# Kernel tuning notes

Measured on AMD Instinct MI355X. Metric: run time of the kernel, lower is better.

Reference implementation:

```python
import jax, jax.numpy as jnp
import numpy as np

B, S, D, H = 2, 2048, 1024, 16
HD = D // H
DFF = 4096
EPS = 1e-5


def layernorm(x, w, b):
    m = jnp.mean(x, axis=-1, keepdims=True)
    v = jnp.mean((x - m) ** 2, axis=-1, keepdims=True)
    return (x - m) / jnp.sqrt(v + EPS) * w + b


def setup_inputs() -> dict:
    key = jax.random.key(0)
    ks = jax.random.split(key, 5)
    s = 0.02  # init scale for weights
    return {
        "src": jax.random.normal(ks[0], (B, S, D), jnp.float32),
        "norm_w": jnp.ones((D,), jnp.float32),
        "norm_b": jnp.zeros((D,), jnp.float32),
        "wqkv_w": jax.random.normal(ks[1], (D, 3 * D), jnp.float32) * s,
        "wqkv_b": jnp.zeros((3 * D,), jnp.float32),
        "out_w": jax.random.normal(ks[2], (D, D), jnp.float32) * s,
        "out_b": jnp.zeros((D,), jnp.float32),
        "fnorm_w": jnp.ones((D,), jnp.float32),
        "fnorm_b": jnp.zeros((D,), jnp.float32),
        "ff1_w": jax.random.normal(ks[3], (D, DFF), jnp.float32) * s,
        "ff1_b": jnp.zeros((DFF,), jnp.float32),
        "ff2_w": jax.random.normal(ks[4], (DFF, D), jnp.float32) * s,
        "ff2_b": jnp.zeros((D,), jnp.float32),
    }


def reference(src, norm_w, norm_b, wqkv_w, wqkv_b, out_w, out_b,
              fnorm_w, fnorm_b, ff1_w, ff1_b, ff2_w, ff2_b):
    bs, seq, dim = src.shape
    hd = dim // H
    qkv = layernorm(src, norm_w, norm_b) @ wqkv_w + wqkv_b  # [b,s,3d]
    qkv = qkv.reshape(bs, seq, 3, H, hd).transpose(2, 0, 3, 1, 4)  # [3,b,h,s,hd]
    q, k, v = qkv[0], qkv[1], qkv[2]
    # ALiBi bias: (j - i) * 2^{-h}, -inf above diagonal (causal)
    i = jnp.arange(seq)[:, None]
    j = jnp.arange(seq)[None, :]
    slopes = 2.0 ** (-jnp.arange(H, dtype=jnp.float32))  # [h]
    rel = (j - i).astype(jnp.float32)  # [s,s]
    bias = slopes[:, None, None] * rel[None]  # [h,s,s]
    bias = jnp.where((j > i)[None], -jnp.inf, bias)
    scale = 1.0 / jnp.sqrt(jnp.asarray(hd, jnp.float32))
    scores = jnp.einsum("bhqd,bhkd->bhqk", q, k) * scale + bias[None]
    attn = jax.nn.softmax(scores, axis=-1)
    ctx = jnp.einsum("bhqk,bhkd->bhqd", attn, v)
    ctx = ctx.transpose(0, 2, 1, 3).reshape(bs, seq, dim)
    src = src + ctx @ out_w + out_b
    h = layernorm(src, fnorm_w, fnorm_b)
    ff = jax.nn.relu(h @ ff1_w + ff1_b) @ ff2_w + ff2_b
    return src + ff
```

## Files before the change

kernel.cpp:

```cpp
#include <hip/hip_runtime.h>
#include <math.h>

#define S_   2048
#define D_   1024
#define H_   16
#define DFF_ 4096

#define NEGINF (-__builtin_huge_valf())

typedef __bf16 bf16x8 __attribute__((ext_vector_type(8)));
typedef float  f32x4  __attribute__((ext_vector_type(4)));

static __device__ __forceinline__ unsigned short f2bf_rne(float f) {
    unsigned int u = __float_as_uint(f);
    u = (u + 0x7fffu + ((u >> 16) & 1u)) >> 16;
    return (unsigned short)u;
}

template<bool OBF>
__global__ __launch_bounds__(256) void ln_kernel(
    const float* __restrict__ x, const float* __restrict__ w,
    const float* __restrict__ b, void* __restrict__ y)
{
    const int row = blockIdx.x;
    const int t = threadIdx.x;
    const float4 v = reinterpret_cast<const float4*>(x + (size_t)row * D_)[t];
    float s  = v.x + v.y + v.z + v.w;
    float ss = v.x*v.x + v.y*v.y + v.z*v.z + v.w*v.w;
    #pragma unroll
    for (int o = 32; o; o >>= 1) {
        s  += __shfl_xor(s,  o, 64);
        ss += __shfl_xor(ss, o, 64);
    }
    __shared__ float red[8];
    const int wid = t >> 6, lane = t & 63;
    if (lane == 0) { red[wid] = s; red[4 + wid] = ss; }
    __syncthreads();
    s  = red[0] + red[1] + red[2] + red[3];
    ss = red[4] + red[5] + red[6] + red[7];
    const float mean = s * (1.f / D_);
    const float var  = ss * (1.f / D_) - mean * mean;
    const float rstd = rsqrtf(var + 1e-5f);
    const float4 wv = reinterpret_cast<const float4*>(w)[t];
    const float4 bv = reinterpret_cast<const float4*>(b)[t];
    float4 o;
    o.x = (v.x - mean) * rstd * wv.x + bv.x;
    o.y = (v.y - mean) * rstd * wv.y + bv.y;
    o.z = (v.z - mean) * rstd * wv.z + bv.z;
    o.w = (v.w - mean) * rstd * wv.w + bv.w;
    if (OBF) {
        ushort4 o4;
        o4.x = f2bf_rne(o.x); o4.y = f2bf_rne(o.y);
        o4.z = f2bf_rne(o.z); o4.w = f2bf_rne(o.w);
        reinterpret_cast<ushort4*>((unsigned short*)y + (size_t)row * D_)[t] = o4;
    } else {
        reinterpret_cast<float4*>((float*)y + (size_t)row * D_)[t] = o;
    }
}

__global__ __launch_bounds__(256) void wcast_kernel(
    const float* __restrict__ in, unsigned short* __restrict__ outT, int K, int N)
{
    __shared__ float t[64][65];
    const int n0 = blockIdx.x * 64, k0 = blockIdx.y * 64;
    const int tid = threadIdx.x;
    #pragma unroll
    for (int i = 0; i < 16; ++i) {
        const int idx = i * 256 + tid;
        const int kk = idx >> 6, nn = idx & 63;
        t[kk][nn] = in[(size_t)(k0 + kk) * N + n0 + nn];
    }
    __syncthreads();
    #pragma unroll
    for (int i = 0; i < 16; ++i) {
        const int idx = i * 256 + tid;
        const int nn = idx >> 6, kk = idx & 63;
        outT[(size_t)(n0 + nn) * K + k0 + kk] = f2bf_rne(t[kk][nn]);
    }
}

template<int EPI, bool OBF>
__global__ __launch_bounds__(256) void bgemm_kernel(
    const __bf16* __restrict__ A,
    const __bf16* __restrict__ Bt,
    const float* __restrict__ bias, const float* __restrict__ res,
    void* __restrict__ Cv, int M, int N, int K)
{
    __shared__ __align__(16) __bf16 As[128 * 64];
    __shared__ __align__(16) __bf16 Bs[128 * 64];
    const int tid  = threadIdx.x;
    const int w    = tid >> 6, lane = tid & 63;
    const int wr   = w >> 1, wc = w & 1;

    const int nwg  = gridDim.x;
    const int lin  = blockIdx.x;
    const int wg   = (lin & 7) * (nwg >> 3) + (lin >> 3);
    const int gridN = N >> 7;
    const int row0 = (wg / gridN) << 7;
    const int col0 = (wg % gridN) << 7;

    const int srow = lane >> 3;
    const int scol = ((lane & 7) ^ srow) << 3;
    const int frow = lane & 15;
    const int l4   = lane >> 4;
    const int r7   = frow & 7;

    f32x4 acc[4][4] = {};

    for (int kt = 0; kt < K; kt += 64) {
        #pragma unroll
        for (int it = 0; it < 4; ++it) {
            const int arow = w * 32 + it * 8;
            __builtin_amdgcn_global_load_lds(
                (__attribute__((address_space(1))) void*)(A + (size_t)(row0 + arow + srow) * K + kt + scol),
                (__attribute__((address_space(3))) void*)(&As[arow * 64]), 16, 0, 0);
            __builtin_amdgcn_global_load_lds(
                (__attribute__((address_space(1))) void*)(Bt + (size_t)(col0 + arow + srow) * K + kt + scol),
                (__attribute__((address_space(3))) void*)(&Bs[arow * 64]), 16, 0, 0);
        }
        __syncthreads();
        #pragma unroll
        for (int kk = 0; kk < 2; ++kk) {
            const int ch = ((kk * 4 + l4) ^ r7) * 8;
            bf16x8 af[4], bfr[4];
            #pragma unroll
            for (int i = 0; i < 4; ++i) {
                af[i]  = *(const bf16x8*)&As[(wr * 64 + i * 16 + frow) * 64 + ch];
                bfr[i] = *(const bf16x8*)&Bs[(wc * 64 + i * 16 + frow) * 64 + ch];
            }
            #pragma unroll
            for (int mi = 0; mi < 4; ++mi)
                #pragma unroll
                for (int ni = 0; ni < 4; ++ni)
                    acc[mi][ni] = __builtin_amdgcn_mfma_f32_16x16x32_bf16(
                        af[mi], bfr[ni], acc[mi][ni], 0, 0, 0);
        }
        __syncthreads();
    }

    float bz[4];
    #pragma unroll
    for (int ni = 0; ni < 4; ++ni) bz[ni] = bias[col0 + wc * 64 + ni * 16 + frow];
    #pragma unroll
    for (int mi = 0; mi < 4; ++mi) {
        #pragma unroll
        for (int j = 0; j < 4; ++j) {
            const int row = row0 + wr * 64 + mi * 16 + l4 * 4 + j;
            #pragma unroll
            for (int ni = 0; ni < 4; ++ni) {
                const int col = col0 + wc * 64 + ni * 16 + frow;
                float v = acc[mi][ni][j] + bz[ni];
                if (EPI == 1) v = fmaxf(v, 0.f);
                if (EPI == 2) v += res[(size_t)row * N + col];
                if (OBF) ((unsigned short*)Cv)[(size_t)row * N + col] = f2bf_rne(v);
                else     ((float*)Cv)[(size_t)row * N + col] = v;
            }
        }
    }
}

__global__ __launch_bounds__(256) void attn_kernel(
    const __bf16* __restrict__ qkv, __bf16* __restrict__ ctx)
{
    const int pair = blockIdx.x & 15;
    const int bh   = blockIdx.x >> 4;
    const int b    = bh >> 4, h = bh & 15;
    const int tid  = threadIdx.x;
    const int wid  = tid >> 6, lane = tid & 63;
    const int l15  = lane & 15, l4 = lane >> 4;
    const float slope = exp2f(-(float)h);
    const size_t rowb = (size_t)b * S_;

    __shared__ __align__(16) __bf16 Ks[64 * 72];
    __shared__ __align__(16) __bf16 Vt[64 * 72];
    __shared__ __align__(16) __bf16 Ps[4 * 16 * 72];

    const int jr = tid >> 3;
    const int c  = tid & 7;
    const int c8 = c * 8;
    __bf16* psw = &Ps[wid * 16 * 72];
    const __bf16* base = qkv + rowb * 3072 + h * 64;

    #pragma unroll 1
    for (int half = 0; half < 2; ++half) {
        const int qt = half ? 31 - pair : pair;
        const int i0 = qt << 6;

        bf16x8 qf[2];
        {
            const __bf16* qp = base + (size_t)(i0 + wid * 16 + l15) * 3072 + l4 * 8;
            qf[0] = *(const bf16x8*)(qp);
            qf[1] = *(const bf16x8*)(qp + 32);
        }

        float m[4], l[4];
        f32x4 acc[4];
        #pragma unroll
        for (int j = 0; j < 4; ++j) { m[j] = NEGINF; l[j] = 0.f; }
        #pragma unroll
        for (int ni = 0; ni < 4; ++ni) acc[ni] = (f32x4){0.f, 0.f, 0.f, 0.f};

        bf16x8 k0, k1, v0, v1;
        {
            const __bf16* kvp = base + (size_t)jr * 3072;
            k0 = *(const bf16x8*)(kvp + 1024 + c8);
            v0 = *(const bf16x8*)(kvp + 2048 + c8);
            k1 = *(const bf16x8*)(kvp + 32 * 3072 + 1024 + c8);
            v1 = *(const bf16x8*)(kvp + 32 * 3072 + 2048 + c8);
        }

        for (int kt = 0; kt <= qt; ++kt) {
            __syncthreads();
            *(bf16x8*)&Ks[jr * 72 + c8]        = k0;
            *(bf16x8*)&Ks[(jr + 32) * 72 + c8] = k1;
            const int sw0 = (((jr >> 3) ^ c) & 7) * 8 + (jr & 7);
            const int sw1 = ((((jr + 32) >> 3) ^ c) & 7) * 8 + (jr & 7);
            #pragma unroll
            for (int e = 0; e < 8; ++e) {
                Vt[(c8 + e) * 72 + sw0] = v0[e];
                Vt[(c8 + e) * 72 + sw1] = v1[e];
            }
            __syncthreads();

            if (kt < qt) {
                const __bf16* kvp = base + (size_t)(((kt + 1) << 6) + jr) * 3072;
                k0 = *(const bf16x8*)(kvp + 1024 + c8);
                v0 = *(const bf16x8*)(kvp + 2048 + c8);
                k1 = *(const bf16x8*)(kvp + 32 * 3072 + 1024 + c8);
                v1 = *(const bf16x8*)(kvp + 32 * 3072 + 2048 + c8);
            }

            f32x4 sf[4];
            #pragma unroll
            for (int ni = 0; ni < 4; ++ni) sf[ni] = (f32x4){0.f, 0.f, 0.f, 0.f};
            #pragma unroll
            for (int kd = 0; kd < 2; ++kd)
                #pragma unroll
                for (int ni = 0; ni < 4; ++ni) {
                    const bf16x8 bf = *(const bf16x8*)&Ks[(ni * 16 + l15) * 72 + kd * 32 + l4 * 8];
                    sf[ni] = __builtin_amdgcn_mfma_f32_16x16x32_bf16(qf[kd], bf, sf[ni], 0, 0, 0);
                }

            float pv[4][4];
            const int j0 = kt << 6;
            if (kt == qt) {
                #pragma unroll
                for (int ni = 0; ni < 4; ++ni) {
                    const int jcol = ni * 16 + l15;
                    #pragma unroll
                    for (int j = 0; j < 4; ++j) {
                        const int iloc = wid * 16 + l4 * 4 + j;
                        pv[ni][j] = (jcol <= iloc)
                            ? fmaf(slope, (float)(jcol - iloc), sf[ni][j] * 0.125f)
                            : NEGINF;
                    }
                }
            } else {
                const float dbase = (float)(j0 - i0);
                #pragma unroll
                for (int ni = 0; ni < 4; ++ni) {
                    const int jcol = ni * 16 + l15;
                    #pragma unroll
                    for (int j = 0; j < 4; ++j) {
                        const int iloc = wid * 16 + l4 * 4 + j;
                        pv[ni][j] = fmaf(slope, dbase + (float)(jcol - iloc), sf[ni][j] * 0.125f);
                    }
                }
            }

            #pragma unroll
            for (int j = 0; j < 4; ++j) {
                float mx = fmaxf(fmaxf(pv[0][j], pv[1][j]), fmaxf(pv[2][j], pv[3][j]));
                mx = fmaxf(mx, __shfl_xor(mx, 1, 64));
                mx = fmaxf(mx, __shfl_xor(mx, 2, 64));
                mx = fmaxf(mx, __shfl_xor(mx, 4, 64));
                mx = fmaxf(mx, __shfl_xor(mx, 8, 64));
                const float mnew = fmaxf(m[j], mx);
                const float corr = __expf(m[j] - mnew);
                float s0 = 0.f;
                #pragma unroll
                for (int ni = 0; ni < 4; ++ni) {
                    const float e = __expf(pv[ni][j] - mnew);
                    pv[ni][j] = e;
                    s0 += e;
                }
                s0 += __shfl_xor(s0, 1, 64);
                s0 += __shfl_xor(s0, 2, 64);
                s0 += __shfl_xor(s0, 4, 64);
                s0 += __shfl_xor(s0, 8, 64);
                l[j] = l[j] * corr + s0;
                m[j] = mnew;
                #pragma unroll
                for (int ni = 0; ni < 4; ++ni) acc[ni][j] *= corr;
            }

            #pragma unroll
            for (int ni = 0; ni < 4; ++ni)
                #pragma unroll
                for (int j = 0; j < 4; ++j)
                    psw[(l4 * 4 + j) * 72 + ni * 16 + l15] = (__bf16)pv[ni][j];
            asm volatile("" ::: "memory");

            #pragma unroll
            for (int kk = 0; kk < 2; ++kk) {
                const bf16x8 pa = *(const bf16x8*)&psw[l15 * 72 + kk * 32 + l4 * 8];
                #pragma unroll
                for (int ni = 0; ni < 4; ++ni) {
                    const int d = ni * 16 + l15;
                    const int pc = ((kk * 4 + l4) ^ (d >> 3)) & 7;
                    const bf16x8 bv = *(const bf16x8*)&Vt[d * 72 + pc * 8];
                    acc[ni] = __builtin_amdgcn_mfma_f32_16x16x32_bf16(pa, bv, acc[ni], 0, 0, 0);
                }
            }
        }

        #pragma unroll
        for (int ni = 0; ni < 4; ++ni) {
            const int col = h * 64 + ni * 16 + l15;
            #pragma unroll
            for (int j = 0; j < 4; ++j) {
                const int row = i0 + wid * 16 + l4 * 4 + j;
                ctx[(rowb + row) * (size_t)D_ + col] = (__bf16)(acc[ni][j] / l[j]);
            }
        }
    }
}

extern "C" void kernel_launch(void* const* d_in, const int* in_sizes, int n_in,
                              void* d_out, int out_size, void* d_ws, size_t ws_size,
                              hipStream_t stream) {
    const float* src     = (const float*)d_in[0];
    const float* norm_w  = (const float*)d_in[1];
    const float* norm_b  = (const float*)d_in[2];
    const float* wqkv_w  = (const float*)d_in[3];
    const float* wqkv_b  = (const float*)d_in[4];
    const float* out_w   = (const float*)d_in[5];
    const float* out_b   = (const float*)d_in[6];
    const float* fnorm_w = (const float*)d_in[7];
    const float* fnorm_b = (const float*)d_in[8];
    const float* ff1_w   = (const float*)d_in[9];
    const float* ff1_b   = (const float*)d_in[10];
    const float* ff2_w   = (const float*)d_in[11];
    const float* ff2_b   = (const float*)d_in[12];
    float* out = (float*)d_out;

    const int M = 2 * S_;
    const size_t MB = 1u << 20;
    char* W = (char*)d_ws;
    unsigned short* wqkvT = (unsigned short*)(W);
    unsigned short* outT  = (unsigned short*)(W + 6  * MB);
    unsigned short* ff1T  = (unsigned short*)(W + 8  * MB);
    unsigned short* ff2T  = (unsigned short*)(W + 16 * MB);
    unsigned short* h1    = (unsigned short*)(W + 24 * MB);
    unsigned short* qkv   = (unsigned short*)(W + 32 * MB);
    unsigned short* ctx   = (unsigned short*)(W + 24 * MB);
    unsigned short* h2    = (unsigned short*)(W + 32 * MB);
    unsigned short* ffmid = (unsigned short*)(W + 40 * MB);
    float*          src2  = (float*)        (W + 80 * MB);

    wcast_kernel<<<dim3(3072/64, 1024/64), 256, 0, stream>>>(wqkv_w, wqkvT, 1024, 3072);
    wcast_kernel<<<dim3(1024/64, 1024/64), 256, 0, stream>>>(out_w,  outT,  1024, 1024);
    wcast_kernel<<<dim3(4096/64, 1024/64), 256, 0, stream>>>(ff1_w,  ff1T,  1024, 4096);
    wcast_kernel<<<dim3(1024/64, 4096/64), 256, 0, stream>>>(ff2_w,  ff2T,  4096, 1024);

    ln_kernel<true><<<M, 256, 0, stream>>>(src, norm_w, norm_b, h1);
    bgemm_kernel<0, true><<<(3072/128) * (M/128), 256, 0, stream>>>(
        (const __bf16*)h1, (const __bf16*)wqkvT, wqkv_b, nullptr, qkv, M, 3072, 1024);
    attn_kernel<<<2 * H_ * 16, 256, 0, stream>>>((const __bf16*)qkv, (__bf16*)ctx);
    bgemm_kernel<2, false><<<(1024/128) * (M/128), 256, 0, stream>>>(
        (const __bf16*)ctx, (const __bf16*)outT, out_b, src, src2, M, 1024, 1024);
    ln_kernel<true><<<M, 256, 0, stream>>>(src2, fnorm_w, fnorm_b, h2);
    bgemm_kernel<1, true><<<(4096/128) * (M/128), 256, 0, stream>>>(
        (const __bf16*)h2, (const __bf16*)ff1T, ff1_b, nullptr, ffmid, M, 4096, 1024);
    bgemm_kernel<2, false><<<(1024/128) * (M/128), 256, 0, stream>>>(
        (const __bf16*)ffmid, (const __bf16*)ff2T, ff2_b, src2, out, M, 1024, 4096);
}
```

Before: 411.1 us.

## Double-buffer GEMM LDS tiles and split attention into one block per query tile

The GEMM now uses two LDS buffers and prefetches the next K tile with global_load_lds while computing on the current one, with a single barrier per iteration. Tile assignment now walks down M first, which changes L2 reuse of weight columns. Attention drops the paired-tile loop and launches 1024 blocks, one per query tile, ordered with the longest causal tiles first to improve load balance and occupancy. Double buffering doubles LDS use per GEMM block (64KB), which may lower occupancy.

```diff
diff --git a/kernel.cpp b/kernel.cpp
--- a/kernel.cpp
+++ b/kernel.cpp
@@ -86,8 +86,8 @@
     const float* __restrict__ bias, const float* __restrict__ res,
     void* __restrict__ Cv, int M, int N, int K)
 {
-    __shared__ __align__(16) __bf16 As[128 * 64];
-    __shared__ __align__(16) __bf16 Bs[128 * 64];
+    __shared__ __align__(16) __bf16 As[2][128 * 64];
+    __shared__ __align__(16) __bf16 Bs[2][128 * 64];
     const int tid  = threadIdx.x;
     const int w    = tid >> 6, lane = tid & 63;
     const int wr   = w >> 1, wc = w & 1;
@@ -95,9 +95,9 @@
     const int nwg  = gridDim.x;
     const int lin  = blockIdx.x;
     const int wg   = (lin & 7) * (nwg >> 3) + (lin >> 3);
-    const int gridN = N >> 7;
-    const int row0 = (wg / gridN) << 7;
-    const int col0 = (wg % gridN) << 7;
+    const int gridM = M >> 7;
+    const int col0 = (wg / gridM) << 7;
+    const int row0 = (wg % gridM) << 7;
 
     const int srow = lane >> 3;
     const int scol = ((lane & 7) ^ srow) << 3;
@@ -105,28 +105,39 @@
     const int l4   = lane >> 4;
     const int r7   = frow & 7;
 
+    const __bf16* Abase = A  + (size_t)(row0 + srow) * K + scol;
+    const __bf16* Bbase = Bt + (size_t)(col0 + srow) * K + scol;
+
     f32x4 acc[4][4] = {};
-
-    for (int kt = 0; kt < K; kt += 64) {
-        #pragma unroll
-        for (int it = 0; it < 4; ++it) {
-            const int arow = w * 32 + it * 8;
-            __builtin_amdgcn_global_load_lds(
-                (__attribute__((address_space(1))) void*)(A + (size_t)(row0 + arow + srow) * K + kt + scol),
-                (__attribute__((address_space(3))) void*)(&As[arow * 64]), 16, 0, 0);
-            __builtin_amdgcn_global_load_lds(
-                (__attribute__((address_space(1))) void*)(Bt + (size_t)(col0 + arow + srow) * K + kt + scol),
-                (__attribute__((address_space(3))) void*)(&Bs[arow * 64]), 16, 0, 0);
-        }
+    const int nt = K >> 6;
+
+#define STAGE_G(bufi, kt)                                                              \
+    _Pragma("unroll")                                                                  \
+    for (int it = 0; it < 4; ++it) {                                                   \
+        const int arow = w * 32 + it * 8;                                              \
+        __builtin_amdgcn_global_load_lds(                                              \
+            (__attribute__((address_space(1))) void*)(Abase + (size_t)arow * K + (kt)),\
+            (__attribute__((address_space(3))) void*)(&As[bufi][arow * 64]), 16, 0, 0);\
+        __builtin_amdgcn_global_load_lds(                                              \
+            (__attribute__((address_space(1))) void*)(Bbase + (size_t)arow * K + (kt)),\
+            (__attribute__((address_space(3))) void*)(&Bs[bufi][arow * 64]), 16, 0, 0);\
+    }
+
+    STAGE_G(0, 0)
+    int buf = 0;
+    for (int t = 0; t < nt; ++t) {
         __syncthreads();
+        if (t + 1 < nt) {
+            STAGE_G(buf ^ 1, (t + 1) << 6)
+        }
         #pragma unroll
         for (int kk = 0; kk < 2; ++kk) {
             const int ch = ((kk * 4 + l4) ^ r7) * 8;
             bf16x8 af[4], bfr[4];
             #pragma unroll
             for (int i = 0; i < 4; ++i) {
-                af[i]  = *(const bf16x8*)&As[(wr * 64 + i * 16 + frow) * 64 + ch];
-                bfr[i] = *(const bf16x8*)&Bs[(wc * 64 + i * 16 + frow) * 64 + ch];
+                af[i]  = *(const bf16x8*)&As[buf][(wr * 64 + i * 16 + frow) * 64 + ch];
+                bfr[i] = *(const bf16x8*)&Bs[buf][(wc * 64 + i * 16 + frow) * 64 + ch];
             }
             #pragma unroll
             for (int mi = 0; mi < 4; ++mi)
@@ -135,8 +146,9 @@
                     acc[mi][ni] = __builtin_amdgcn_mfma_f32_16x16x32_bf16(
                         af[mi], bfr[ni], acc[mi][ni], 0, 0, 0);
         }
-        __syncthreads();
-    }
+        buf ^= 1;
+    }
+#undef STAGE_G
 
     float bz[4];
     #pragma unroll
@@ -162,8 +174,8 @@
 __global__ __launch_bounds__(256) void attn_kernel(
     const __bf16* __restrict__ qkv, __bf16* __restrict__ ctx)
 {
-    const int pair = blockIdx.x & 15;
-    const int bh   = blockIdx.x >> 4;
+    const int bh   = blockIdx.x & 31;
+    const int qt   = 31 - (blockIdx.x >> 5);
     const int b    = bh >> 4, h = bh & 15;
     const int tid  = threadIdx.x;
     const int wid  = tid >> 6, lane = tid & 63;
@@ -181,147 +193,143 @@
     __bf16* psw = &Ps[wid * 16 * 72];
     const __bf16* base = qkv + rowb * 3072 + h * 64;
 
-    #pragma unroll 1
-    for (int half = 0; half < 2; ++half) {
-        const int qt = half ? 31 - pair : pair;
-        const int i0 = qt << 6;
-
-        bf16x8 qf[2];
-        {
-            const __bf16* qp = base + (size_t)(i0 + wid * 16 + l15) * 3072 + l4 * 8;
-            qf[0] = *(const bf16x8*)(qp);
-            qf[1] = *(const bf16x8*)(qp + 32);
-        }
-
-        float m[4], l[4];
-        f32x4 acc[4];
-        #pragma unroll
-        for (int j = 0; j < 4; ++j) { m[j] = NEGINF; l[j] = 0.f; }
-        #pragma unroll
-        for (int ni = 0; ni < 4; ++ni) acc[ni] = (f32x4){0.f, 0.f, 0.f, 0.f};
-
-        bf16x8 k0, k1, v0, v1;
-        {
-            const __bf16* kvp = base + (size_t)jr * 3072;
+    const int i0 = qt << 6;
+
+    bf16x8 qf[2];
+    {
+        const __bf16* qp = base + (size_t)(i0 + wid * 16 + l15) * 3072 + l4 * 8;
+        qf[0] = *(const bf16x8*)(qp);
+        qf[1] = *(const bf16x8*)(qp + 32);
+    }
+
+    float m[4], l[4];
+    f32x4 acc[4];
+    #pragma unroll
+    for (int j = 0; j < 4; ++j) { m[j] = NEGINF; l[j] = 0.f; }
+    #pragma unroll
+    for (int ni = 0; ni < 4; ++ni) acc[ni] = (f32x4){0.f, 0.f, 0.f, 0.f};
+
+    bf16x8 k0, k1, v0, v1;
+    {
+        const __bf16* kvp = base + (size_t)jr * 3072;
+        k0 = *(const bf16x8*)(kvp + 1024 + c8);
+        v0 = *(const bf16x8*)(kvp + 2048 + c8);
+        k1 = *(const bf16x8*)(kvp + 32 * 3072 + 1024 + c8);
+        v1 = *(const bf16x8*)(kvp + 32 * 3072 + 2048 + c8);
+    }
+
+    for (int kt = 0; kt <= qt; ++kt) {
+        __syncthreads();
+        *(bf16x8*)&Ks[jr * 72 + c8]        = k0;
+        *(bf16x8*)&Ks[(jr + 32) * 72 + c8] = k1;
+        const int sw0 = (((jr >> 3) ^ c) & 7) * 8 + (jr & 7);
+        const int sw1 = ((((jr + 32) >> 3) ^ c) & 7) * 8 + (jr & 7);
+        #pragma unroll
+        for (int e = 0; e < 8; ++e) {
+            Vt[(c8 + e) * 72 + sw0] = v0[e];
+            Vt[(c8 + e) * 72 + sw1] = v1[e];
+        }
+        __syncthreads();
+
+        if (kt < qt) {
+            const __bf16* kvp = base + (size_t)(((kt + 1) << 6) + jr) * 3072;
             k0 = *(const bf16x8*)(kvp + 1024 + c8);
             v0 = *(const bf16x8*)(kvp + 2048 + c8);
             k1 = *(const bf16x8*)(kvp + 32 * 3072 + 1024 + c8);
             v1 = *(const bf16x8*)(kvp + 32 * 3072 + 2048 + c8);
         }
 
-        for (int kt = 0; kt <= qt; ++kt) {
-            __syncthreads();
-            *(bf16x8*)&Ks[jr * 72 + c8]        = k0;
-            *(bf16x8*)&Ks[(jr + 32) * 72 + c8] = k1;
-            const int sw0 = (((jr >> 3) ^ c) & 7) * 8 + (jr & 7);
-            const int sw1 = ((((jr + 32) >> 3) ^ c) & 7) * 8 + (jr & 7);
-            #pragma unroll
-            for (int e = 0; e < 8; ++e) {
-                Vt[(c8 + e) * 72 + sw0] = v0[e];
-                Vt[(c8 + e) * 72 + sw1] = v1[e];
-            }
-            __syncthreads();
-
-            if (kt < qt) {
-                const __bf16* kvp = base + (size_t)(((kt + 1) << 6) + jr) * 3072;
-                k0 = *(const bf16x8*)(kvp + 1024 + c8);
-                v0 = *(const bf16x8*)(kvp + 2048 + c8);
-                k1 = *(const bf16x8*)(kvp + 32 * 3072 + 1024 + c8);
-                v1 = *(const bf16x8*)(kvp + 32 * 3072 + 2048 + c8);
-            }
-
-            f32x4 sf[4];
-            #pragma unroll
-            for (int ni = 0; ni < 4; ++ni) sf[ni] = (f32x4){0.f, 0.f, 0.f, 0.f};
-            #pragma unroll
-            for (int kd = 0; kd < 2; ++kd)
+        f32x4 sf[4];
+        #pragma unroll
+        for (int ni = 0; ni < 4; ++ni) sf[ni] = (f32x4){0.f, 0.f, 0.f, 0.f};
+        #pragma unroll
+        for (int kd = 0; kd < 2; ++kd)
+            #pragma unroll
+            for (int ni = 0; ni < 4; ++ni) {
+                const bf16x8 bf = *(const bf16x8*)&Ks[(ni * 16 + l15) * 72 + kd * 32 + l4 * 8];
+                sf[ni] = __builtin_amdgcn_mfma_f32_16x16x32_bf16(qf[kd], bf, sf[ni], 0, 0, 0);
+            }
+
+        float pv[4][4];
+        const int j0 = kt << 6;
+        if (kt == qt) {
+            #pragma unroll
+            for (int ni = 0; ni < 4; ++ni) {
+                const int jcol = ni * 16 + l15;
                 #pragma unroll
-                for (int ni = 0; ni < 4; ++ni) {
-                    const bf16x8 bf = *(const bf16x8*)&Ks[(ni * 16 + l15) * 72 + kd * 32 + l4 * 8];
-                    sf[ni] = __builtin_amdgcn_mfma_f32_16x16x32_bf16(qf[kd], bf, sf[ni], 0, 0, 0);
+                for (int j = 0; j < 4; ++j) {
+                    const int iloc = wid * 16 + l4 * 4 + j;
+                    pv[ni][j] = (jcol <= iloc)
+                        ? fmaf(slope, (float)(jcol - iloc), sf[ni][j] * 0.125f)
+                        : NEGINF;
                 }
-
-            float pv[4][4];
-            const int j0 = kt << 6;
-            if (kt == qt) {
+            }
+        } else {
+            const float dbase = (float)(j0 - i0);
+            #pragma unroll
+            for (int ni = 0; ni < 4; ++ni) {
+                const int jcol = ni * 16 + l15;
                 #pragma unroll
-                for (int ni = 0; ni < 4; ++ni) {
-                    const int jcol = ni * 16 + l15;
-                    #pragma unroll
-                    for (int j = 0; j < 4; ++j) {
-                        const int iloc = wid * 16 + l4 * 4 + j;
-                        pv[ni][j] = (jcol <= iloc)
-                            ? fmaf(slope, (float)(jcol - iloc), sf[ni][j] * 0.125f)
-                            : NEGINF;
-                    }
+                for (int j = 0; j < 4; ++j) {
+                    const int iloc = wid * 16 + l4 * 4 + j;
+                    pv[ni][j] = fmaf(slope, dbase + (float)(jcol - iloc), sf[ni][j] * 0.125f);
                 }
-            } else {
-                const float dbase = (float)(j0 - i0);
-                #pragma unroll
-                for (int ni = 0; ni < 4; ++ni) {
-                    const int jcol = ni * 16 + l15;
-                    #pragma unroll
-                    for (int j = 0; j < 4; ++j) {
-                        const int iloc = wid * 16 + l4 * 4 + j;
-                        pv[ni][j] = fmaf(slope, dbase + (float)(jcol - iloc), sf[ni][j] * 0.125f);
-                    }
-                }
-            }
-
-            #pragma unroll
-            for (int j = 0; j < 4; ++j) {
-                float mx = fmaxf(fmaxf(pv[0][j], pv[1][j]), fmaxf(pv[2][j], pv[3][j]));
-                mx = fmaxf(mx, __shfl_xor(mx, 1, 64));
-                mx = fmaxf(mx, __shfl_xor(mx, 2, 64));
-                mx = fmaxf(mx, __shfl_xor(mx, 4, 64));
-                mx = fmaxf(mx, __shfl_xor(mx, 8, 64));
-                const float mnew = fmaxf(m[j], mx);
-                const float corr = __expf(m[j] - mnew);
-                float s0 = 0.f;
-                #pragma unroll
-                for (int ni = 0; ni < 4; ++ni) {
-                    const float e = __expf(pv[ni][j] - mnew);
-                    pv[ni][j] = e;
-                    s0 += e;
-                }
-                s0 += __shfl_xor(s0, 1, 64);
-                s0 += __shfl_xor(s0, 2, 64);
-                s0 += __shfl_xor(s0, 4, 64);
-                s0 += __shfl_xor(s0, 8, 64);
-                l[j] = l[j] * corr + s0;
-                m[j] = mnew;
-                #pragma unroll
-                for (int ni = 0; ni < 4; ++ni) acc[ni][j] *= corr;
-            }
-
-            #pragma unroll
-            for (int ni = 0; ni < 4; ++ni)
-                #pragma unroll
-                for (int j = 0; j < 4; ++j)
-                    psw[(l4 * 4 + j) * 72 + ni * 16 + l15] = (__bf16)pv[ni][j];
-            asm volatile("" ::: "memory");
-
-            #pragma unroll
-            for (int kk = 0; kk < 2; ++kk) {
-                const bf16x8 pa = *(const bf16x8*)&psw[l15 * 72 + kk * 32 + l4 * 8];
-                #pragma unroll
-                for (int ni = 0; ni < 4; ++ni) {
-                    const int d = ni * 16 + l15;
-                    const int pc = ((kk * 4 + l4) ^ (d >> 3)) & 7;
-                    const bf16x8 bv = *(const bf16x8*)&Vt[d * 72 + pc * 8];
-                    acc[ni] = __builtin_amdgcn_mfma_f32_16x16x32_bf16(pa, bv, acc[ni], 0, 0, 0);
-                }
-            }
-        }
-
-        #pragma unroll
-        for (int ni = 0; ni < 4; ++ni) {
-            const int col = h * 64 + ni * 16 + l15;
-            #pragma unroll
-            for (int j = 0; j < 4; ++j) {
-                const int row = i0 + wid * 16 + l4 * 4 + j;
-                ctx[(rowb + row) * (size_t)D_ + col] = (__bf16)(acc[ni][j] / l[j]);
-            }
+            }
+        }
+
+        #pragma unroll
+        for (int j = 0; j < 4; ++j) {
+            float mx = fmaxf(fmaxf(pv[0][j], pv[1][j]), fmaxf(pv[2][j], pv[3][j]));
+            mx = fmaxf(mx, __shfl_xor(mx, 1, 64));
+            mx = fmaxf(mx, __shfl_xor(mx, 2, 64));
+            mx = fmaxf(mx, __shfl_xor(mx, 4, 64));
+            mx = fmaxf(mx, __shfl_xor(mx, 8, 64));
+            const float mnew = fmaxf(m[j], mx);
+            const float corr = __expf(m[j] - mnew);
+            float s0 = 0.f;
+            #pragma unroll
+            for (int ni = 0; ni < 4; ++ni) {
+                const float e = __expf(pv[ni][j] - mnew);
+                pv[ni][j] = e;
+                s0 += e;
+            }
+            s0 += __shfl_xor(s0, 1, 64);
+            s0 += __shfl_xor(s0, 2, 64);
+            s0 += __shfl_xor(s0, 4, 64);
+            s0 += __shfl_xor(s0, 8, 64);
+            l[j] = l[j] * corr + s0;
+            m[j] = mnew;
+            #pragma unroll
+            for (int ni = 0; ni < 4; ++ni) acc[ni][j] *= corr;
+        }
+
+        #pragma unroll
+        for (int ni = 0; ni < 4; ++ni)
+            #pragma unroll
+            for (int j = 0; j < 4; ++j)
+                psw[(l4 * 4 + j) * 72 + ni * 16 + l15] = (__bf16)pv[ni][j];
+        asm volatile("" ::: "memory");
+
+        #pragma unroll
+        for (int kk = 0; kk < 2; ++kk) {
+            const bf16x8 pa = *(const bf16x8*)&psw[l15 * 72 + kk * 32 + l4 * 8];
+            #pragma unroll
+            for (int ni = 0; ni < 4; ++ni) {
+                const int d = ni * 16 + l15;
+                const int pc = ((kk * 4 + l4) ^ (d >> 3)) & 7;
+                const bf16x8 bv = *(const bf16x8*)&Vt[d * 72 + pc * 8];
+                acc[ni] = __builtin_amdgcn_mfma_f32_16x16x32_bf16(pa, bv, acc[ni], 0, 0, 0);
+            }
+        }
+    }
+
+    #pragma unroll
+    for (int ni = 0; ni < 4; ++ni) {
+        const int col = h * 64 + ni * 16 + l15;
+        #pragma unroll
+        for (int j = 0; j < 4; ++j) {
+            const int row = i0 + wid * 16 + l4 * 4 + j;
+            ctx[(rowb + row) * (size_t)D_ + col] = (__bf16)(acc[ni][j] / l[j]);
         }
     }
 }
@@ -366,7 +374,7 @@
     ln_kernel<true><<<M, 256, 0, stream>>>(src, norm_w, norm_b, h1);
     bgemm_kernel<0, true><<<(3072/128) * (M/128), 256, 0, stream>>>(
         (const __bf16*)h1, (const __bf16*)wqkvT, wqkv_b, nullptr, qkv, M, 3072, 1024);
-    attn_kernel<<<2 * H_ * 16, 256, 0, stream>>>((const __bf16*)qkv, (__bf16*)ctx);
+    attn_kernel<<<1024, 256, 0, stream>>>((const __bf16*)qkv, (__bf16*)ctx);
     bgemm_kernel<2, false><<<(1024/128) * (M/128), 256, 0, stream>>>(
         (const __bf16*)ctx, (const __bf16*)outT, out_b, src, src2, M, 1024, 1024);
     ln_kernel<true><<<M, 256, 0, stream>>>(src2, fnorm_w, fnorm_b, h2);
```

Measured after the change: 394.6 us. 4.0% less time.
